# Kernel optimization log

Hardware: AMD Instinct MI355X
Metric: run time of the kernel (lower is better)

## Reference

```python
import jax, jax.numpy as jnp
import numpy as np

N, E = 3072, 49152
C_IN, HID, C_OUT = 16, 64, 3
KS = (2000, 1000, 500)  # ceil(pool_ratio * n_nodes) per depth: 2000/3072, 0.5, 0.5


def gcn(x, A, W, b):
    # GCNConv(improved=True) with edge weights: A_hat = A + 2I,
    # out = D^-1/2 A_hat D^-1/2 (x W) + b
    n = A.shape[0]
    i = jnp.arange(n)
    A_hat = A.at[i, i].add(2.0)
    deg = A_hat.sum(axis=1)
    dis = jnp.where(deg > 0, 1.0 / jnp.sqrt(deg), 0.0)
    return (dis[:, None] * A_hat * dis[None, :]) @ (x @ W) + b


def augment(A):
    # GraphUNet.augment_adj: remove self loops, add self loops (w=1),
    # spspmm(A, A) -> A^2, remove self loops. Dense equivalent.
    n = A.shape[0]
    i = jnp.arange(n)
    A1 = A.at[i, i].set(1.0)
    A2 = A1 @ A1
    return A2.at[i, i].set(0.0)


def topk_pool(x, A, p, k):
    # TopKPooling: score = tanh((x . p)/||p||), keep top-k nodes, scale features
    score = jnp.tanh((x @ p) / jnp.linalg.norm(p))
    _, perm = jax.lax.top_k(score, k)
    x = x[perm] * score[perm][:, None]
    return x, A[perm][:, perm], perm


def setup_inputs():
    key = jax.random.key(0)
    ks = jax.random.split(key, 16)
    g = lambda k, shape, s=1.0: jax.random.normal(k, shape, dtype=jnp.float32) * s
    s = 0.1
    return {
        "x": g(ks[0], (N, C_IN)),
        "edge_index": jax.random.randint(ks[1], (2, E), 0, N),
        "Wd0": g(ks[2], (C_IN, HID), s), "bd0": jnp.zeros((HID,), jnp.float32),
        "Wd1": g(ks[3], (HID, HID), s), "bd1": jnp.zeros((HID,), jnp.float32),
        "Wd2": g(ks[4], (HID, HID), s), "bd2": jnp.zeros((HID,), jnp.float32),
        "Wd3": g(ks[5], (HID, HID), s), "bd3": jnp.zeros((HID,), jnp.float32),
        "p1": g(ks[6], (HID,), s), "p2": g(ks[7], (HID,), s), "p3": g(ks[8], (HID,), s),
        "Wu0": g(ks[9], (HID, HID), s), "bu0": jnp.zeros((HID,), jnp.float32),
        "Wu1": g(ks[10], (HID, HID), s), "bu1": jnp.zeros((HID,), jnp.float32),
        "Wu2": g(ks[11], (HID, C_OUT), s), "bu2": jnp.zeros((C_OUT,), jnp.float32),
    }


def reference(x, edge_index, Wd0, bd0, Wd1, bd1, Wd2, bd2, Wd3, bd3,
              p1, p2, p3, Wu0, bu0, Wu1, bu1, Wu2, bu2):
    # eval mode: dropout_edge(p=0.2) and F.dropout(p=0.92) are identity
    # dense weighted adjacency; duplicate edges sum, matching sparse scatter-add
    A = jnp.zeros((N, N), jnp.float32).at[edge_index[0], edge_index[1]].add(1.0)
    x = jax.nn.relu(gcn(x, A, Wd0, bd0))
    xs, adjs, perms = [x], [A], []
    for i, (W, b, p) in enumerate(((Wd1, bd1, p1), (Wd2, bd2, p2), (Wd3, bd3, p3))):
        A = augment(A)
        x, A, perm = topk_pool(x, A, p, KS[i])
        x = jax.nn.relu(gcn(x, A, W, b))
        if i < 2:
            xs.append(x)
            adjs.append(A)
        perms.append(perm)
    for i, (W, b) in enumerate(((Wu0, bu0), (Wu1, bu1), (Wu2, bu2))):
        j = 2 - i
        res, Aj, perm = xs[j], adjs[j], perms[j]
        up = jnp.zeros_like(res).at[perm].set(x)  # unpool
        x = gcn(res + up, Aj, W, b)  # sum_res=True skip connection
        if i < 2:
            x = jax.nn.relu(x)
    return jax.nn.softmax(x, axis=1)
```

## Files before the change

kernel.cpp:

```cpp
#include <hip/hip_runtime.h>
#include <hip/hip_bf16.h>
#include <cstdint>
#include <cstddef>
#include <math.h>


#define DIVUP(a,b) (((a)+(b)-1)/(b))

using s16x8 = __attribute__((ext_vector_type(8))) short;
using f32x4 = __attribute__((ext_vector_type(4))) float;
using l64x2 = __attribute__((ext_vector_type(2))) long;

template<int N> __device__ __forceinline__ void waitvm() {
    if constexpr (N == 0)       asm volatile("s_waitcnt vmcnt(0)" ::: "memory");
    else if constexpr (N == 2)  asm volatile("s_waitcnt vmcnt(2)" ::: "memory");
    else if constexpr (N == 4)  asm volatile("s_waitcnt vmcnt(4)" ::: "memory");
    else if constexpr (N == 8)  asm volatile("s_waitcnt vmcnt(8)" ::: "memory");
    else                        asm volatile("s_waitcnt vmcnt(16)" ::: "memory");
}

__device__ __forceinline__ unsigned short f2bf(float v) {
    union { float f; unsigned u; } a; a.f = v;
    unsigned u = a.u;
    u = u + 0x7FFFu + ((u >> 16) & 1u);
    return (unsigned short)(u >> 16);
}
__device__ __forceinline__ float bf2f(unsigned short h) {
    union { unsigned u; float f; } a; a.u = ((unsigned)h) << 16; return a.f;
}
__device__ __forceinline__ unsigned char f2e4m3(float v) {
    if (v <= 0.f) return 0;
    int e = 0; float m = v;
    while (m >= 2.f) { m *= 0.5f; ++e; }
    int mant = (int)(m * 8.f + 0.5f) - 8;
    if (mant >= 8) { mant = 0; ++e; }
    return (unsigned char)(((e + 7) << 3) | mant);
}
__device__ __forceinline__ int perm64(int x) {
    return ((x >> 3) & 3) * 16 + ((x >> 5) & 1) * 8 + (x & 7);
}
__device__ __forceinline__ void gload_lds16(const unsigned short* g, unsigned short* l) {
    __builtin_amdgcn_global_load_lds(
        (const __attribute__((address_space(1))) void*)g,
        (__attribute__((address_space(3))) void*)l, 16, 0, 0);
}
__device__ __forceinline__ void gload_lds16b(const unsigned char* g, unsigned char* l) {
    __builtin_amdgcn_global_load_lds(
        (const __attribute__((address_space(1))) void*)g,
        (__attribute__((address_space(3))) void*)l, 16, 0, 0);
}


__global__ void k_scatter(const int* __restrict__ e, float* __restrict__ A, int E, int n) {
    int t = blockIdx.x * blockDim.x + threadIdx.x;
    if (t < E) atomicAdd(&A[(size_t)e[t] * n + e[E + t]], 1.0f);
}

__global__ void k_a0_plane(const float* __restrict__ A, unsigned short* __restrict__ H,
                           unsigned char* __restrict__ F8,
                           float* __restrict__ d0, float* __restrict__ dsum, int n) {
    int t = blockIdx.x * 256 + threadIdx.x;
    int i = t / n, j = t - i * n;
    float v = A[t];
    if (i == j) { d0[i] = v; v = 1.0f; }
    H[t] = f2bf(v);
    F8[(size_t)i * n + (j & ~63) + perm64(j & 63)] = f2e4m3(v);
    __shared__ float red[256];
    red[threadIdx.x] = v; __syncthreads();
    for (int o = 128; o > 0; o >>= 1) {
        if (threadIdx.x < o) red[threadIdx.x] += red[threadIdx.x + o];
        __syncthreads();
    }
    if (threadIdx.x == 0) atomicAdd(&dsum[i], red[0]);
}

__global__ void k_transpose_i8(const unsigned char* __restrict__ S, unsigned char* __restrict__ D, int n) {
    __shared__ unsigned char tile[64][65];
    int bx = blockIdx.x * 64, by = blockIdx.y * 64;
    const int tx = threadIdx.x & 63, ty = threadIdx.x >> 6;
    #pragma unroll
    for (int dy = 0; dy < 64; dy += 4)
        tile[ty + dy][tx] = S[(size_t)(by + ty + dy) * n + bx + perm64(tx)];
    __syncthreads();
    #pragma unroll
    for (int dy = 0; dy < 64; dy += 4)
        D[(size_t)(bx + ty + dy) * n + by + perm64(tx)] = tile[tx][ty + dy];
}

__global__ void k_disv(const float* __restrict__ dsum, const float* __restrict__ diag,
                       float* __restrict__ dis, int n) {
    int i = blockIdx.x * blockDim.x + threadIdx.x;
    if (i >= n) return;
    float deg = dsum[i] + 1.0f + (diag ? diag[i] : 0.0f);
    dis[i] = deg > 0.f ? 1.0f / sqrtf(deg) : 0.f;
}

__global__ void k_scores(const float* __restrict__ x, const float* __restrict__ pv,
                         float* __restrict__ sc, int n) {
    __shared__ float pl[64];
    if (threadIdx.x < 64) pl[threadIdx.x] = pv[threadIdx.x];
    __syncthreads();
    float n2 = 0.f;
    #pragma unroll
    for (int k = 0; k < 64; ++k) n2 += pl[k] * pl[k];
    float nrm = sqrtf(n2);
    int i = blockIdx.x * blockDim.x + threadIdx.x;
    if (i >= n) return;
    const float* xr = x + (size_t)i * 64;
    float d = 0.f;
    #pragma unroll
    for (int k = 0; k < 64; ++k) d += xr[k] * pl[k];
    sc[i] = tanhf(d / nrm);
}

__global__ void k_count_rank(const float* __restrict__ score, int* __restrict__ rank, int n) {
    __shared__ float ls[256];
    const int i = blockIdx.x * 256 + threadIdx.x;
    const int j0 = blockIdx.y * 256;
    int jj_n = n - j0; if (jj_n > 256) jj_n = 256;
    ls[threadIdx.x] = (j0 + threadIdx.x < n) ? score[j0 + threadIdx.x] : -INFINITY;
    __syncthreads();
    if (i >= n) return;
    const float si = score[i];
    int cnt = 0;
    for (int jj = 0; jj < jj_n; ++jj) {
        float sj = ls[jj];
        int j = j0 + jj;
        cnt += (sj > si) || (sj == si && j < i);
    }
    atomicAdd(&rank[i], cnt);
}

__global__ void k_topk_finish(const float* __restrict__ score, const int* __restrict__ rank,
                              const float* __restrict__ x, int n, int k, int kp,
                              int* __restrict__ perm, float* __restrict__ scout,
                              float* __restrict__ xo) {
    int i = blockIdx.x * blockDim.x + threadIdx.x;
    if (i < n) {
        int r = rank[i];
        if (r < k) {
            float s = score[i];
            perm[r] = i; scout[r] = s;
            const float* xr = x + (size_t)i * 64;
            float* xw = xo + (size_t)r * 64;
            #pragma unroll 8
            for (int f = 0; f < 64; ++f) xw[f] = xr[f] * s;
        }
    }
    if (i >= k && i < kp) { perm[i] = 0; scout[i] = 0.f; }
}

__global__ void k_unpool(const float* __restrict__ res, const float* __restrict__ xc,
                         const int* __restrict__ rank, float* __restrict__ o, int n, int k) {
    int t = blockIdx.x * blockDim.x + threadIdx.x;
    if (t >= n * 64) return;
    int r = rank[t >> 6];
    o[t] = res[t] + (r < k ? xc[(size_t)r * 64 + (t & 63)] : 0.f);
}

__global__ void k_xw(const float* __restrict__ x, const float* __restrict__ W,
                     const float* __restrict__ dis, int n, int np, int cin, int ldw, int nout,
                     float* __restrict__ Y, unsigned short* __restrict__ T0,
                     unsigned short* __restrict__ T1, unsigned short* __restrict__ T2) {
    int t = blockIdx.x * blockDim.x + threadIdx.x;
    if (t >= np * 64) return;
    int i = t >> 6, f = t & 63;
    float y = 0.f;
    if (i < n && f < nout) {
        float a = 0.f;
        for (int k = 0; k < cin; ++k) a += x[(size_t)i * cin + k] * W[(size_t)k * ldw + f];
        y = dis[i] * a;
    }
    Y[t] = y;
    unsigned short h0 = f2bf(y);
    float r1 = y - bf2f(h0);
    unsigned short h1 = f2bf(r1);
    float r2 = r1 - bf2f(h1);
    size_t ti = (size_t)f * np + i;
    T0[ti] = h0; T1[ti] = h1; T2[ti] = f2bf(r2);
}


template<int TM>
__global__ __launch_bounds__(256) void k_aug8(
    const unsigned char* __restrict__ P8, const unsigned char* __restrict__ Q8,
    const int* __restrict__ perm, int kk, int kp, int K, int ns,
    unsigned short* __restrict__ H0, unsigned short* __restrict__ T0,
    float* __restrict__ dsum)
{
    constexpr int BM = TM * 32;
    constexpr int PS = BM * 64;
    constexpr int D = 3;
    constexpr int STG = 2 * PS;
    constexpr int LPP = TM / 2;
    constexpr int LPS = 2 * LPP;
    constexpr int TRE = BM * (BM + 2) * 2;
    constexpr int SMEB = (D * STG > TRE) ? D * STG : TRE;
    __shared__ __align__(16) unsigned char smem[SMEB];
    const int tid = threadIdx.x, lane = tid & 63;
    const int wm = tid >> 7, wn = (tid >> 6) & 1;
    const int bm = blockIdx.x * BM, bn = blockIdx.y * BM;
    const unsigned char* spA[LPP];
    const unsigned char* spB[LPP];
    int dstb[LPP];
    #pragma unroll
    for (int it = 0; it < LPP; ++it) {
        int s = tid + it * 256;
        int row = s >> 2, c = (s & 3) ^ ((row >> 1) & 3);
        dstb[it] = (s - lane) * 16;
        spA[it] = P8 + (size_t)perm[bm + row] * ns + 16 * c;
        spB[it] = Q8 + (size_t)perm[bn + row] * ns + 16 * c;
    }
    f32x4 acc[TM][TM] = {};
    const int l15 = lane & 15, kb = lane >> 4;
    const int nt = K >> 6;

    auto stage = [&](int b, int koff) {
        unsigned char* base = smem + b * STG;
        #pragma unroll
        for (int it = 0; it < LPP; ++it) gload_lds16b(spA[it] + koff, base + dstb[it]);
        #pragma unroll
        for (int it = 0; it < LPP; ++it) gload_lds16b(spB[it] + koff, base + PS + dstb[it]);
    };
    auto compute = [&](int b) {
        const unsigned char* base = smem + b * STG;
        l64x2 av[TM], bv[TM];
        #pragma unroll
        for (int mi = 0; mi < TM; ++mi) {
            int row = wm * (TM * 16) + mi * 16 + l15;
            int slot = kb ^ ((row >> 1) & 3);
            av[mi] = *(const l64x2*)(base + row * 64 + slot * 16);
        }
        #pragma unroll
        for (int ni = 0; ni < TM; ++ni) {
            int row = wn * (TM * 16) + ni * 16 + l15;
            int slot = kb ^ ((row >> 1) & 3);
            bv[ni] = *(const l64x2*)(base + PS + row * 64 + slot * 16);
        }
        #pragma unroll
        for (int h = 0; h < 2; ++h)
            #pragma unroll
            for (int mi = 0; mi < TM; ++mi)
                #pragma unroll
                for (int ni = 0; ni < TM; ++ni)
                    acc[mi][ni] = __builtin_amdgcn_mfma_f32_16x16x32_fp8_fp8(
                        av[mi][h], bv[ni][h], acc[mi][ni], 0, 0, 0);
    };

    stage(0, 0); stage(1, 64);
    for (int t = 0; t < nt; ++t) {
        const int ahead = nt - 1 - t;
        if (ahead >= D - 1) {
            stage((t + D - 1) % D, (t + D - 1) * 64);
            waitvm<2 * LPS>();
        } else if (ahead == 1) {
            waitvm<LPS>();
        } else {
            waitvm<0>();
        }
        __builtin_amdgcn_sched_barrier(0);
        __builtin_amdgcn_s_barrier();
        compute(t % D);
        __builtin_amdgcn_s_barrier();
    }

    const int hi = lane >> 4;
    #pragma unroll
    for (int mi = 0; mi < TM; ++mi)
        #pragma unroll
        for (int r = 0; r < 4; ++r) {
            int row = bm + wm * (TM * 16) + mi * 16 + hi * 4 + r;
            float s = 0.f;
            #pragma unroll
            for (int ni = 0; ni < TM; ++ni) {
                int col = bn + wn * (TM * 16) + ni * 16 + l15;
                float v = (row < kk && col < kk) ? ((row == col) ? 1.f : acc[mi][ni][r]) : 0.f;
                H0[(size_t)row * kp + col] = f2bf(v);
                s += v;
            }
            #pragma unroll
            for (int m = 1; m < 16; m <<= 1) s += __shfl_xor(s, m);
            if (l15 == 0) atomicAdd(&dsum[row], s);
        }

    unsigned short* smw = (unsigned short*)smem;
    __syncthreads();
    #pragma unroll
    for (int mi = 0; mi < TM; ++mi)
        #pragma unroll
        for (int ni = 0; ni < TM; ++ni)
            #pragma unroll
            for (int r = 0; r < 4; ++r) {
                int rl = wm * (TM * 16) + mi * 16 + hi * 4 + r;
                int cl = wn * (TM * 16) + ni * 16 + l15;
                int row = bm + rl, col = bn + cl;
                float v = (row < kk && col < kk) ? ((row == col) ? 1.f : acc[mi][ni][r]) : 0.f;
                smw[rl * (BM + 2) + cl] = f2bf(v);
            }
    __syncthreads();
    #pragma unroll
    for (int e = 0; e < BM * BM / 256; ++e) {
        int idx = tid + e * 256;
        int j = idx / BM, i = idx & (BM - 1);
        T0[(size_t)(bn + j) * kp + (bm + i)] = smw[i * (BM + 2) + j];
    }
}

template<int TM, int PA, int PB, int NP, int NT>
__global__ __launch_bounds__(256) void k_aug2(
    const unsigned short* __restrict__ Pa, const unsigned short* __restrict__ Pb,
    const unsigned short* __restrict__ Qa, const unsigned short* __restrict__ Qb,
    const int* __restrict__ perm, int kk, int kp, int K, int ns,
    unsigned short* __restrict__ H0, unsigned short* __restrict__ H1,
    unsigned short* __restrict__ H2,
    unsigned short* __restrict__ T0, unsigned short* __restrict__ T1,
    float* __restrict__ dsum)
{
    constexpr int BM  = TM * 32;
    constexpr int PS  = TM * 2048;
    constexpr int D   = 3;
    constexpr int STG = (PA + PB) * PS;
    constexpr int LPS = TM * (PA + PB);
    constexpr int TRE = NT ? (BM * (BM + 2)) : 0;
    constexpr int SME = (D * STG > TRE) ? (D * STG) : TRE;
    __shared__ __align__(16) unsigned short smem[SME];
    const int tid = threadIdx.x, lane = tid & 63;
    const int wm = tid >> 7, wn = (tid >> 6) & 1;
    const int bm = blockIdx.x * BM, bn = blockIdx.y * BM;
    const unsigned short* P[2] = {Pa, Pb};
    const unsigned short* Q[2] = {Qa, Qb};
    const unsigned short* sp[PA][TM];
    const unsigned short* sq[PB][TM];
    int dst[TM];
    #pragma unroll
    for (int it = 0; it < TM; ++it) {
        int s = tid + it * 256;
        int row = s >> 3, c = (s & 7) ^ (row & 7);
        dst[it] = (s - lane) * 8;
        #pragma unroll
        for (int p = 0; p < PA; ++p)
            sp[p][it] = P[p] + (size_t)perm[bm + row] * ns + 8 * c;
        #pragma unroll
        for (int p = 0; p < PB; ++p)
            sq[p][it] = Q[p] + (size_t)perm[bn + row] * ns + 8 * c;
    }
    f32x4 acc[TM][TM] = {};
    const int l15 = lane & 15, kb = lane >> 4;
    const int nt = K >> 6;

    auto stage = [&](int b, int koff) {
        unsigned short* base = smem + b * STG;
        #pragma unroll
        for (int p = 0; p < PA; ++p)
            #pragma unroll
            for (int it = 0; it < TM; ++it)
                gload_lds16(sp[p][it] + koff, base + p * PS + dst[it]);
        #pragma unroll
        for (int p = 0; p < PB; ++p)
            #pragma unroll
            for (int it = 0; it < TM; ++it)
                gload_lds16(sq[p][it] + koff, base + PA * PS + p * PS + dst[it]);
    };
    auto compute = [&](int b) {
        const unsigned short* base = smem + b * STG;
        #pragma unroll
        for (int h = 0; h < 2; ++h) {
            s16x8 av[PA][TM], bv[PB][TM];
            #pragma unroll
            for (int p = 0; p < PA; ++p)
                #pragma unroll
                for (int mi = 0; mi < TM; ++mi) {
                    int row = wm * (TM * 16) + mi * 16 + l15;
                    int slot = (h * 4 + kb) ^ (row & 7);
                    av[p][mi] = *(const s16x8*)(base + p * PS + row * 64 + slot * 8);
                }
            #pragma unroll
            for (int p = 0; p < PB; ++p)
                #pragma unroll
                for (int ni = 0; ni < TM; ++ni) {
                    int row = wn * (TM * 16) + ni * 16 + l15;
                    int slot = (h * 4 + kb) ^ (row & 7);
                    bv[p][ni] = *(const s16x8*)(base + PA * PS + p * PS + row * 64 + slot * 8);
                }
            #pragma unroll
            for (int mi = 0; mi < TM; ++mi)
                #pragma unroll
                for (int ni = 0; ni < TM; ++ni)
                    #pragma unroll
                    for (int pa = 0; pa < PA; ++pa)
                        #pragma unroll
                        for (int pb = 0; pb < PB; ++pb)
                            acc[mi][ni] = __builtin_amdgcn_mfma_f32_16x16x32_bf16(
                                av[pa][mi], bv[pb][ni], acc[mi][ni], 0, 0, 0);
        }
    };

    for (int i = 0; i < D - 1; ++i) stage(i, i * 64);
    for (int t = 0; t < nt; ++t) {
        const int ahead = nt - 1 - t;
        if (ahead >= D - 1) {
            stage((t + D - 1) % D, (t + D - 1) * 64);
            waitvm<2 * LPS>();
        } else if (ahead == 1) {
            waitvm<LPS>();
        } else {
            waitvm<0>();
        }
        __builtin_amdgcn_sched_barrier(0);
        __builtin_amdgcn_s_barrier();
        compute(t % D);
        __builtin_amdgcn_s_barrier();
    }

    const int hi = lane >> 4;
    #pragma unroll
    for (int mi = 0; mi < TM; ++mi)
        #pragma unroll
        for (int r = 0; r < 4; ++r) {
            int row = bm + wm * (TM * 16) + mi * 16 + hi * 4 + r;
            float s = 0.f;
            #pragma unroll
            for (int ni = 0; ni < TM; ++ni) {
                int col = bn + wn * (TM * 16) + ni * 16 + l15;
                float v = (row < kk && col < kk) ? ((row == col) ? 1.f : acc[mi][ni][r]) : 0.f;
                s += v;
                unsigned short h0 = f2bf(v);
                size_t o = (size_t)row * kp + col;
                H0[o] = h0;
                if (NP > 1) {
                    float r1 = v - bf2f(h0);
                    unsigned short h1 = f2bf(r1);
                    H1[o] = h1;
                    if (NP > 2) H2[o] = f2bf(r1 - bf2f(h1));
                }
            }
            #pragma unroll
            for (int m = 1; m < 16; m <<= 1) s += __shfl_xor(s, m);
            if (l15 == 0) atomicAdd(&dsum[row], s);
        }

    if (NT > 0) {
        #pragma unroll
        for (int pass = 0; pass < NT; ++pass) {
            __syncthreads();
            #pragma unroll
            for (int mi = 0; mi < TM; ++mi)
                #pragma unroll
                for (int ni = 0; ni < TM; ++ni)
                    #pragma unroll
                    for (int r = 0; r < 4; ++r) {
                        int rl = wm * (TM * 16) + mi * 16 + hi * 4 + r;
                        int cl = wn * (TM * 16) + ni * 16 + l15;
                        int row = bm + rl, col = bn + cl;
                        float v = (row < kk && col < kk) ? ((row == col) ? 1.f : acc[mi][ni][r]) : 0.f;
                        unsigned short h0 = f2bf(v);
                        unsigned short hv = h0;
                        if (pass == 1) hv = f2bf(v - bf2f(h0));
                        smem[rl * (BM + 2) + cl] = hv;
                    }
            __syncthreads();
            unsigned short* T = pass ? T1 : T0;
            #pragma unroll
            for (int e = 0; e < BM * BM / 256; ++e) {
                int idx = tid + e * 256;
                int j = idx / BM, i = idx & (BM - 1);
                T[(size_t)(bn + j) * kp + (bm + i)] = smem[i * (BM + 2) + j];
            }
        }
    }
}

template<int PA>
__global__ __launch_bounds__(256) void k_gcn_gemm(
    const unsigned short* __restrict__ Aa, const unsigned short* __restrict__ Ab,
    const unsigned short* __restrict__ Ac,
    const unsigned short* __restrict__ B0, const unsigned short* __restrict__ B1,
    const unsigned short* __restrict__ B2,
    int np, int kchunk, float* __restrict__ Zp)
{
    __shared__ __align__(16) unsigned short la[PA * 4096];
    __shared__ __align__(16) unsigned short lb[3 * 4096];
    const int tid = threadIdx.x, lane = tid & 63, wv = tid >> 6;
    const int bm = blockIdx.x * 64;
    const int kbeg = blockIdx.y * kchunk;
    const unsigned short* A[3] = {Aa, Ab, Ac};
    const unsigned short* B[3] = {B0, B1, B2};
    const unsigned short* sa[PA][2];
    const unsigned short* sb[3][2];
    int dst[2];
    #pragma unroll
    for (int it = 0; it < 2; ++it) {
        int s = tid + it * 256;
        int row = s >> 3, c = (s & 7) ^ (row & 7);
        dst[it] = (s - lane) * 8;
        #pragma unroll
        for (int p = 0; p < PA; ++p)
            sa[p][it] = A[p] + (size_t)(bm + row) * np + kbeg + 8 * c;
        #pragma unroll
        for (int p = 0; p < 3; ++p)
            sb[p][it] = B[p] + (size_t)row * np + kbeg + 8 * c;
    }
    f32x4 acc[4] = {};
    const int l15 = lane & 15, kb = lane >> 4;
    const int nt = kchunk >> 6;

    for (int tt = 0; tt < nt; ++tt) {
        if (tt) __syncthreads();
        int koff = tt * 64;
        #pragma unroll
        for (int p = 0; p < PA; ++p)
            #pragma unroll
            for (int it = 0; it < 2; ++it)
                gload_lds16(sa[p][it] + koff, &la[p * 4096 + dst[it]]);
        #pragma unroll
        for (int p = 0; p < 3; ++p)
            #pragma unroll
            for (int it = 0; it < 2; ++it)
                gload_lds16(sb[p][it] + koff, &lb[p * 4096 + dst[it]]);
        __syncthreads();
        #pragma unroll
        for (int h = 0; h < 2; ++h) {
            s16x8 av[PA], bv[3][4];
            #pragma unroll
            for (int p = 0; p < PA; ++p) {
                int row = wv * 16 + l15;
                int slot = (h * 4 + kb) ^ (row & 7);
                av[p] = *(const s16x8*)&la[p * 4096 + row * 64 + slot * 8];
            }
            #pragma unroll
            for (int p = 0; p < 3; ++p)
                #pragma unroll
                for (int ni = 0; ni < 4; ++ni) {
                    int row = ni * 16 + l15;
                    int slot = (h * 4 + kb) ^ (row & 7);
                    bv[p][ni] = *(const s16x8*)&lb[p * 4096 + row * 64 + slot * 8];
                }
            #pragma unroll
            for (int ni = 0; ni < 4; ++ni)
                #pragma unroll
                for (int pa = 0; pa < PA; ++pa)
                    #pragma unroll
                    for (int pb = 0; pb <= 2 - pa; ++pb)
                        acc[ni] = __builtin_amdgcn_mfma_f32_16x16x32_bf16(
                            av[pa], bv[pb][ni], acc[ni], 0, 0, 0);
        }
    }

    const int l4 = lane >> 4;
    float* Z = Zp + (size_t)blockIdx.y * np * 64;
    for (int ni = 0; ni < 4; ++ni)
        #pragma unroll
        for (int r = 0; r < 4; ++r) {
            int row = bm + wv * 16 + l4 * 4 + r;
            Z[(size_t)row * 64 + ni * 16 + l15] = acc[ni][r];
        }
}

__global__ void k_gcn_epi(const float* __restrict__ Zp, const float* __restrict__ Y,
                          const float* __restrict__ dis, const float* __restrict__ diagv,
                          const float* __restrict__ b, int n, int np, int nout, int relu,
                          int S, float* __restrict__ xo) {
    int t = blockIdx.x * blockDim.x + threadIdx.x;
    if (t >= n * 64) return;
    int i = t >> 6, f = t & 63;
    float s = 0.f;
    for (int kq = 0; kq < S; ++kq) s += Zp[(size_t)kq * np * 64 + t];
    float coef = 1.f + (diagv ? diagv[i] : 0.f);
    float v = dis[i] * (s + coef * Y[t]) + (f < nout ? b[f] : 0.f);
    if (relu) v = fmaxf(v, 0.f);
    xo[t] = v;
}

__global__ void k_softmax(const float* __restrict__ lg, float* __restrict__ o, int n) {
    int i = blockIdx.x * blockDim.x + threadIdx.x;
    if (i >= n) return;
    float a = lg[i * 64], b = lg[i * 64 + 1], c = lg[i * 64 + 2];
    float m = fmaxf(a, fmaxf(b, c));
    float ea = expf(a - m), eb = expf(b - m), ec = expf(c - m);
    float s = ea + eb + ec;
    o[i * 3] = ea / s; o[i * 3 + 1] = eb / s; o[i * 3 + 2] = ec / s;
}


extern "C" void kernel_launch(void* const* d_in, const int* in_sizes, int n_in,
                              void* d_out, int out_size, void* d_ws, size_t ws_size,
                              hipStream_t stream) {
    const int N0 = 3072;
    const int E = in_sizes[1] / 2;
    const int CIN = in_sizes[0] / N0;

    const float* x_in = (const float*)d_in[0];
    const int*   eidx = (const int*)d_in[1];
    const float* Wd0 = (const float*)d_in[2];  const float* bd0 = (const float*)d_in[3];
    const float* Wd1 = (const float*)d_in[4];  const float* bd1 = (const float*)d_in[5];
    const float* Wd2 = (const float*)d_in[6];  const float* bd2 = (const float*)d_in[7];
    const float* Wd3 = (const float*)d_in[8];  const float* bd3 = (const float*)d_in[9];
    const float* p1  = (const float*)d_in[10]; const float* p2  = (const float*)d_in[11];
    const float* p3  = (const float*)d_in[12];
    const float* Wu0 = (const float*)d_in[13]; const float* bu0 = (const float*)d_in[14];
    const float* Wu1 = (const float*)d_in[15]; const float* bu1 = (const float*)d_in[16];
    const float* Wu2 = (const float*)d_in[17]; const float* bu2 = (const float*)d_in[18];
    float* out = (float*)d_out;

    char* ws = (char*)d_ws;
    size_t off = 0;
    auto alloc = [&](size_t bytes) -> void* {
        off = (off + 255) & ~(size_t)255;
        void* p = ws + off;
        off += bytes;
        return p;
    };

    unsigned short* A0H  = (unsigned short*)alloc((size_t)3072 * 3072 * 2);
    unsigned char*  A0F8 = (unsigned char*)alloc((size_t)3072 * 3072);
    unsigned char*  A0T8 = (unsigned char*)alloc((size_t)3072 * 3072);
    float* d0   = (float*)alloc(3072 * 4);
    float* dis0 = (float*)alloc(3072 * 4);
    float* x0   = (float*)alloc((size_t)3072 * 64 * 4);
    unsigned short* P1H = (unsigned short*)alloc((size_t)2048 * 2048 * 2);
    unsigned short* P1T = (unsigned short*)alloc((size_t)2048 * 2048 * 2);
    float* dis1 = (float*)alloc(2048 * 4);
    float* x1   = (float*)alloc((size_t)2048 * 64 * 4);
    float* xp1  = (float*)alloc((size_t)2048 * 64 * 4);
    unsigned short* P2H  = (unsigned short*)alloc((size_t)1024 * 1024 * 2);
    unsigned short* P2L  = (unsigned short*)alloc((size_t)1024 * 1024 * 2);
    unsigned short* P2TH = (unsigned short*)alloc((size_t)1024 * 1024 * 2);
    unsigned short* P2TL = (unsigned short*)alloc((size_t)1024 * 1024 * 2);
    float* dis2 = (float*)alloc(1024 * 4);
    float* x2   = (float*)alloc((size_t)1024 * 64 * 4);
    float* xp2  = (float*)alloc((size_t)1024 * 64 * 4);
    unsigned short* P3a = (unsigned short*)alloc((size_t)512 * 512 * 2);
    unsigned short* P3b = (unsigned short*)alloc((size_t)512 * 512 * 2);
    unsigned short* P3c = (unsigned short*)alloc((size_t)512 * 512 * 2);
    float* dis3 = (float*)alloc(512 * 4);
    float* x3   = (float*)alloc((size_t)512 * 64 * 4);
    float* xp3  = (float*)alloc((size_t)512 * 64 * 4);
    int*   perm1 = (int*)alloc(2048 * 4);  float* sc1 = (float*)alloc(2048 * 4);
    int*   perm2 = (int*)alloc(1024 * 4);  float* sc2 = (float*)alloc(1024 * 4);
    int*   perm3 = (int*)alloc(512 * 4);   float* sc3 = (float*)alloc(512 * 4);
    float* score = (float*)alloc(3072 * 4);
    float* dsum0 = (float*)alloc(3072 * 4);
    float* dsum1 = (float*)alloc(2048 * 4);
    float* dsum2 = (float*)alloc(1024 * 4);
    float* dsum3 = (float*)alloc(512 * 4);
    int* rank1 = (int*)alloc(3072 * 4);
    int* rank2 = (int*)alloc(2048 * 4);
    int* rank3 = (int*)alloc(1024 * 4);
    float* Yf  = (float*)alloc((size_t)3072 * 64 * 4);
    unsigned short* Yt0 = (unsigned short*)alloc((size_t)64 * 3072 * 2);
    unsigned short* Yt1 = (unsigned short*)alloc((size_t)64 * 3072 * 2);
    unsigned short* Yt2 = (unsigned short*)alloc((size_t)64 * 3072 * 2);
    float* Zp   = (float*)alloc((size_t)8 * 3072 * 64 * 4);
    float* xlog = (float*)alloc((size_t)3072 * 64 * 4);
    float* t2b  = (float*)alloc((size_t)1024 * 64 * 4);
    float* t1b  = (float*)alloc((size_t)2048 * 64 * 4);
    float* t0b  = (float*)alloc((size_t)3072 * 64 * 4);
    char* scratch = (char*)alloc((size_t)3072 * 3072 * 4);
    if (off > ws_size) return;

    float* A0f = (float*)scratch;

    auto gcn = [&](const float* xin, int cin, const float* W, int ldw, int nout, const float* bias,
                   const unsigned short* Pa, const unsigned short* Pb2, const unsigned short* Pc,
                   int PA, int n, int np2, const float* dis, const float* diagv, int relu, float* xout) {
        k_xw<<<DIVUP(np2 * 64, 256), 256, 0, stream>>>(xin, W, dis, n, np2, cin, ldw, nout, Yf, Yt0, Yt1, Yt2);
        int S = (np2 == 1024) ? 16 : 8;
        int kch = np2 / S;
        dim3 gg(np2 / 64, S);
        if (PA == 1)      k_gcn_gemm<1><<<gg, 256, 0, stream>>>(Pa, Pa, Pa, Yt0, Yt1, Yt2, np2, kch, Zp);
        else if (PA == 2) k_gcn_gemm<2><<<gg, 256, 0, stream>>>(Pa, Pb2, Pb2, Yt0, Yt1, Yt2, np2, kch, Zp);
        else              k_gcn_gemm<3><<<gg, 256, 0, stream>>>(Pa, Pb2, Pc, Yt0, Yt1, Yt2, np2, kch, Zp);
        k_gcn_epi<<<DIVUP(n * 64, 256), 256, 0, stream>>>(Zp, Yf, dis, diagv, bias, n, np2, nout, relu, S, xout);
    };

    auto topk = [&](const float* x, const float* pvec, int n, int k, int kp,
                    int* rank, int* perm, float* scv, float* xo) {
        k_scores<<<DIVUP(n, 256), 256, 0, stream>>>(x, pvec, score, n);
        dim3 gr(DIVUP(n, 256), DIVUP(n, 256));
        k_count_rank<<<gr, 256, 0, stream>>>(score, rank, n);
        k_topk_finish<<<DIVUP(n, 256), 256, 0, stream>>>(score, rank, x, n, k, kp, perm, scv, xo);
    };

    hipMemsetAsync(dsum0, 0, (char*)(rank3 + 1024) - (char*)dsum0, stream);

    hipMemsetAsync(A0f, 0, (size_t)3072 * 3072 * 4, stream);
    k_scatter<<<DIVUP(E, 256), 256, 0, stream>>>(eidx, A0f, E, N0);
    k_a0_plane<<<3072 * 3072 / 256, 256, 0, stream>>>(A0f, A0H, A0F8, d0, dsum0, N0);
    k_transpose_i8<<<dim3(48, 48), 256, 0, stream>>>(A0F8, A0T8, 3072);
    k_disv<<<DIVUP(3072, 256), 256, 0, stream>>>(dsum0, d0, dis0, 3072);

    gcn(x_in, CIN, Wd0, 64, 64, bd0, A0H, A0H, A0H, 1, 3072, 3072, dis0, d0, 1, x0);

    topk(x0, p1, 3072, 2000, 2048, rank1, perm1, sc1, xp1);
    k_aug8<2><<<dim3(32, 32), 256, 0, stream>>>(
        A0F8, A0T8, perm1, 2000, 2048, 3072, 3072, P1H, P1T, dsum1);
    k_disv<<<DIVUP(2048, 256), 256, 0, stream>>>(dsum1, nullptr, dis1, 2048);
    gcn(xp1, 64, Wd1, 64, 64, bd1, P1H, P1H, P1H, 1, 2000, 2048, dis1, nullptr, 1, x1);

    topk(x1, p2, 2000, 1000, 1024, rank2, perm2, sc2, xp2);
    k_aug2<2, 1, 1, 2, 2><<<dim3(16, 16), 256, 0, stream>>>(
        P1H, P1H, P1T, P1T, perm2, 1000, 1024, 2048, 2048, P2H, P2L, P2L, P2TH, P2TL, dsum2);
    k_disv<<<DIVUP(1024, 256), 256, 0, stream>>>(dsum2, nullptr, dis2, 1024);
    gcn(xp2, 64, Wd2, 64, 64, bd2, P2H, P2L, P2L, 2, 1000, 1024, dis2, nullptr, 1, x2);

    topk(x2, p3, 1000, 500, 512, rank3, perm3, sc3, xp3);
    k_aug2<2, 2, 2, 3, 0><<<dim3(8, 8), 256, 0, stream>>>(
        P2H, P2L, P2TH, P2TL, perm3, 500, 512, 1024, 1024, P3a, P3b, P3c, nullptr, nullptr, dsum3);
    k_disv<<<DIVUP(512, 256), 256, 0, stream>>>(dsum3, nullptr, dis3, 512);
    gcn(xp3, 64, Wd3, 64, 64, bd3, P3a, P3b, P3c, 3, 500, 512, dis3, nullptr, 1, x3);

    k_unpool<<<DIVUP(1000 * 64, 256), 256, 0, stream>>>(x2, x3, rank3, t2b, 1000, 500);
    gcn(t2b, 64, Wu0, 64, 64, bu0, P2H, P2L, P2L, 2, 1000, 1024, dis2, nullptr, 1, xp2);

    k_unpool<<<DIVUP(2000 * 64, 256), 256, 0, stream>>>(x1, xp2, rank2, t1b, 2000, 1000);
    gcn(t1b, 64, Wu1, 64, 64, bu1, P1H, P1H, P1H, 1, 2000, 2048, dis1, nullptr, 1, xp1);

    k_unpool<<<DIVUP(3072 * 64, 256), 256, 0, stream>>>(x0, xp1, rank1, t0b, 3072, 2000);
    gcn(t0b, 64, Wu2, 3, 3, bu2, A0H, A0H, A0H, 1, 3072, 3072, dis0, d0, 0, xlog);

    k_softmax<<<DIVUP(3072, 256), 256, 0, stream>>>(xlog, out, 3072);
}
```

Measured before the change: 393.7 us.

## Fuse score and degree-normalization kernels into consumers, raise GCN split-K to 16

Removes the k_disv launches by computing D^-1/2 inline in k_xw and k_gcn_epi from dsum/diag, and removes k_scores by recomputing the tanh score inside k_count_rank and k_topk_finish. It also raises the split-K factor to 16 for the 2048 and 3072 GCN GEMMs, enlarging the Zp partial buffer. The aim is fewer small kernel launches and better GEMM occupancy, at the cost of redundant dot-product recomputation in the rank kernel and more partial-sum traffic in the epilogue.

```diff
diff --git a/kernel.cpp b/kernel.cpp
--- a/kernel.cpp
+++ b/kernel.cpp
@@ -38,6 +38,10 @@
 }
 __device__ __forceinline__ int perm64(int x) {
     return ((x >> 3) & 3) * 16 + ((x >> 5) & 1) * 8 + (x & 7);
+}
+__device__ __forceinline__ float disv(const float* dsum, const float* diag, int i) {
+    float deg = dsum[i] + 1.0f + (diag ? diag[i] : 0.0f);
+    return deg > 0.f ? 1.0f / sqrtf(deg) : 0.f;
 }
 __device__ __forceinline__ void gload_lds16(const unsigned short* g, unsigned short* l) {
     __builtin_amdgcn_global_load_lds(
@@ -87,61 +91,68 @@
         D[(size_t)(bx + ty + dy) * n + by + perm64(tx)] = tile[tx][ty + dy];
 }
 
-__global__ void k_disv(const float* __restrict__ dsum, const float* __restrict__ diag,
-                       float* __restrict__ dis, int n) {
-    int i = blockIdx.x * blockDim.x + threadIdx.x;
+__global__ void k_count_rank(const float* __restrict__ x, const float* __restrict__ pv,
+                             int* __restrict__ rank, int n) {
+    __shared__ float pl[64];
+    __shared__ float ls[256];
+    if (threadIdx.x < 64) pl[threadIdx.x] = pv[threadIdx.x];
+    __syncthreads();
+    float n2 = 0.f;
+    #pragma unroll
+    for (int k = 0; k < 64; ++k) n2 += pl[k] * pl[k];
+    const float nrm = sqrtf(n2);
+    const int i = blockIdx.x * 256 + threadIdx.x;
+    const int j = blockIdx.y * 256 + threadIdx.x;
+    float sj = -INFINITY;
+    if (j < n) {
+        const float* xr = x + (size_t)j * 64;
+        float d = 0.f;
+        #pragma unroll
+        for (int k = 0; k < 64; ++k) d += xr[k] * pl[k];
+        sj = tanhf(d / nrm);
+    }
+    ls[threadIdx.x] = sj;
+    __syncthreads();
     if (i >= n) return;
-    float deg = dsum[i] + 1.0f + (diag ? diag[i] : 0.0f);
-    dis[i] = deg > 0.f ? 1.0f / sqrtf(deg) : 0.f;
-}
-
-__global__ void k_scores(const float* __restrict__ x, const float* __restrict__ pv,
-                         float* __restrict__ sc, int n) {
+    float si;
+    {
+        const float* xr = x + (size_t)i * 64;
+        float d = 0.f;
+        #pragma unroll
+        for (int k = 0; k < 64; ++k) d += xr[k] * pl[k];
+        si = tanhf(d / nrm);
+    }
+    const int j0 = blockIdx.y * 256;
+    int jj_n = n - j0; if (jj_n > 256) jj_n = 256;
+    int cnt = 0;
+    for (int jj = 0; jj < jj_n; ++jj) {
+        float s2 = ls[jj];
+        cnt += (s2 > si) || (s2 == si && (j0 + jj) < i);
+    }
+    atomicAdd(&rank[i], cnt);
+}
+
+__global__ void k_topk_finish(const float* __restrict__ x, const float* __restrict__ pv,
+                              const int* __restrict__ rank, int n, int k, int kp,
+                              int* __restrict__ perm, float* __restrict__ scout,
+                              float* __restrict__ xo) {
     __shared__ float pl[64];
     if (threadIdx.x < 64) pl[threadIdx.x] = pv[threadIdx.x];
     __syncthreads();
     float n2 = 0.f;
     #pragma unroll
-    for (int k = 0; k < 64; ++k) n2 += pl[k] * pl[k];
-    float nrm = sqrtf(n2);
-    int i = blockIdx.x * blockDim.x + threadIdx.x;
-    if (i >= n) return;
-    const float* xr = x + (size_t)i * 64;
-    float d = 0.f;
-    #pragma unroll
-    for (int k = 0; k < 64; ++k) d += xr[k] * pl[k];
-    sc[i] = tanhf(d / nrm);
-}
-
-__global__ void k_count_rank(const float* __restrict__ score, int* __restrict__ rank, int n) {
-    __shared__ float ls[256];
-    const int i = blockIdx.x * 256 + threadIdx.x;
-    const int j0 = blockIdx.y * 256;
-    int jj_n = n - j0; if (jj_n > 256) jj_n = 256;
-    ls[threadIdx.x] = (j0 + threadIdx.x < n) ? score[j0 + threadIdx.x] : -INFINITY;
-    __syncthreads();
-    if (i >= n) return;
-    const float si = score[i];
-    int cnt = 0;
-    for (int jj = 0; jj < jj_n; ++jj) {
-        float sj = ls[jj];
-        int j = j0 + jj;
-        cnt += (sj > si) || (sj == si && j < i);
-    }
-    atomicAdd(&rank[i], cnt);
-}
-
-__global__ void k_topk_finish(const float* __restrict__ score, const int* __restrict__ rank,
-                              const float* __restrict__ x, int n, int k, int kp,
-                              int* __restrict__ perm, float* __restrict__ scout,
-                              float* __restrict__ xo) {
+    for (int kq = 0; kq < 64; ++kq) n2 += pl[kq] * pl[kq];
+    const float nrm = sqrtf(n2);
     int i = blockIdx.x * blockDim.x + threadIdx.x;
     if (i < n) {
         int r = rank[i];
         if (r < k) {
-            float s = score[i];
+            const float* xr = x + (size_t)i * 64;
+            float d = 0.f;
+            #pragma unroll
+            for (int kq = 0; kq < 64; ++kq) d += xr[kq] * pl[kq];
+            float s = tanhf(d / nrm);
             perm[r] = i; scout[r] = s;
-            const float* xr = x + (size_t)i * 64;
             float* xw = xo + (size_t)r * 64;
             #pragma unroll 8
             for (int f = 0; f < 64; ++f) xw[f] = xr[f] * s;
@@ -159,7 +170,8 @@
 }
 
 __global__ void k_xw(const float* __restrict__ x, const float* __restrict__ W,
-                     const float* __restrict__ dis, int n, int np, int cin, int ldw, int nout,
+                     const float* __restrict__ dsum, const float* __restrict__ diag,
+                     int n, int np, int cin, int ldw, int nout,
                      float* __restrict__ Y, unsigned short* __restrict__ T0,
                      unsigned short* __restrict__ T1, unsigned short* __restrict__ T2) {
     int t = blockIdx.x * blockDim.x + threadIdx.x;
@@ -169,7 +181,7 @@
     if (i < n && f < nout) {
         float a = 0.f;
         for (int k = 0; k < cin; ++k) a += x[(size_t)i * cin + k] * W[(size_t)k * ldw + f];
-        y = dis[i] * a;
+        y = disv(dsum, diag, i) * a;
     }
     Y[t] = y;
     unsigned short h0 = f2bf(y);
@@ -557,7 +569,7 @@
 }
 
 __global__ void k_gcn_epi(const float* __restrict__ Zp, const float* __restrict__ Y,
-                          const float* __restrict__ dis, const float* __restrict__ diagv,
+                          const float* __restrict__ dsum, const float* __restrict__ diagv,
                           const float* __restrict__ b, int n, int np, int nout, int relu,
                           int S, float* __restrict__ xo) {
     int t = blockIdx.x * blockDim.x + threadIdx.x;
@@ -566,7 +578,7 @@
     float s = 0.f;
     for (int kq = 0; kq < S; ++kq) s += Zp[(size_t)kq * np * 64 + t];
     float coef = 1.f + (diagv ? diagv[i] : 0.f);
-    float v = dis[i] * (s + coef * Y[t]) + (f < nout ? b[f] : 0.f);
+    float v = disv(dsum, diagv, i) * (s + coef * Y[t]) + (f < nout ? b[f] : 0.f);
     if (relu) v = fmaxf(v, 0.f);
     xo[t] = v;
 }
@@ -615,30 +627,25 @@
     unsigned char*  A0F8 = (unsigned char*)alloc((size_t)3072 * 3072);
     unsigned char*  A0T8 = (unsigned char*)alloc((size_t)3072 * 3072);
     float* d0   = (float*)alloc(3072 * 4);
-    float* dis0 = (float*)alloc(3072 * 4);
     float* x0   = (float*)alloc((size_t)3072 * 64 * 4);
     unsigned short* P1H = (unsigned short*)alloc((size_t)2048 * 2048 * 2);
     unsigned short* P1T = (unsigned short*)alloc((size_t)2048 * 2048 * 2);
-    float* dis1 = (float*)alloc(2048 * 4);
     float* x1   = (float*)alloc((size_t)2048 * 64 * 4);
     float* xp1  = (float*)alloc((size_t)2048 * 64 * 4);
     unsigned short* P2H  = (unsigned short*)alloc((size_t)1024 * 1024 * 2);
     unsigned short* P2L  = (unsigned short*)alloc((size_t)1024 * 1024 * 2);
     unsigned short* P2TH = (unsigned short*)alloc((size_t)1024 * 1024 * 2);
     unsigned short* P2TL = (unsigned short*)alloc((size_t)1024 * 1024 * 2);
-    float* dis2 = (float*)alloc(1024 * 4);
     float* x2   = (float*)alloc((size_t)1024 * 64 * 4);
     float* xp2  = (float*)alloc((size_t)1024 * 64 * 4);
     unsigned short* P3a = (unsigned short*)alloc((size_t)512 * 512 * 2);
     unsigned short* P3b = (unsigned short*)alloc((size_t)512 * 512 * 2);
     unsigned short* P3c = (unsigned short*)alloc((size_t)512 * 512 * 2);
-    float* dis3 = (float*)alloc(512 * 4);
     float* x3   = (float*)alloc((size_t)512 * 64 * 4);
     float* xp3  = (float*)alloc((size_t)512 * 64 * 4);
     int*   perm1 = (int*)alloc(2048 * 4);  float* sc1 = (float*)alloc(2048 * 4);
     int*   perm2 = (int*)alloc(1024 * 4);  float* sc2 = (float*)alloc(1024 * 4);
     int*   perm3 = (int*)alloc(512 * 4);   float* sc3 = (float*)alloc(512 * 4);
-    float* score = (float*)alloc(3072 * 4);
     float* dsum0 = (float*)alloc(3072 * 4);
     float* dsum1 = (float*)alloc(2048 * 4);
     float* dsum2 = (float*)alloc(1024 * 4);
@@ -650,7 +657,7 @@
     unsigned short* Yt0 = (unsigned short*)alloc((size_t)64 * 3072 * 2);
     unsigned short* Yt1 = (unsigned short*)alloc((size_t)64 * 3072 * 2);
     unsigned short* Yt2 = (unsigned short*)alloc((size_t)64 * 3072 * 2);
-    float* Zp   = (float*)alloc((size_t)8 * 3072 * 64 * 4);
+    float* Zp   = (float*)alloc((size_t)16 * 3072 * 64 * 4);
     float* xlog = (float*)alloc((size_t)3072 * 64 * 4);
     float* t2b  = (float*)alloc((size_t)1024 * 64 * 4);
     float* t1b  = (float*)alloc((size_t)2048 * 64 * 4);
@@ -662,23 +669,22 @@
 
     auto gcn = [&](const float* xin, int cin, const float* W, int ldw, int nout, const float* bias,
                    const unsigned short* Pa, const unsigned short* Pb2, const unsigned short* Pc,
-                   int PA, int n, int np2, const float* dis, const float* diagv, int relu, float* xout) {
-        k_xw<<<DIVUP(np2 * 64, 256), 256, 0, stream>>>(xin, W, dis, n, np2, cin, ldw, nout, Yf, Yt0, Yt1, Yt2);
-        int S = (np2 == 1024) ? 16 : 8;
+                   int PA, int n, int np2, const float* dsum, const float* diagv, int relu, float* xout) {
+        k_xw<<<DIVUP(np2 * 64, 256), 256, 0, stream>>>(xin, W, dsum, diagv, n, np2, cin, ldw, nout, Yf, Yt0, Yt1, Yt2);
+        int S = (np2 >= 1024) ? 16 : 8;
         int kch = np2 / S;
         dim3 gg(np2 / 64, S);
         if (PA == 1)      k_gcn_gemm<1><<<gg, 256, 0, stream>>>(Pa, Pa, Pa, Yt0, Yt1, Yt2, np2, kch, Zp);
         else if (PA == 2) k_gcn_gemm<2><<<gg, 256, 0, stream>>>(Pa, Pb2, Pb2, Yt0, Yt1, Yt2, np2, kch, Zp);
         else              k_gcn_gemm<3><<<gg, 256, 0, stream>>>(Pa, Pb2, Pc, Yt0, Yt1, Yt2, np2, kch, Zp);
-        k_gcn_epi<<<DIVUP(n * 64, 256), 256, 0, stream>>>(Zp, Yf, dis, diagv, bias, n, np2, nout, relu, S, xout);
+        k_gcn_epi<<<DIVUP(n * 64, 256), 256, 0, stream>>>(Zp, Yf, dsum, diagv, bias, n, np2, nout, relu, S, xout);
     };
 
     auto topk = [&](const float* x, const float* pvec, int n, int k, int kp,
                     int* rank, int* perm, float* scv, float* xo) {
-        k_scores<<<DIVUP(n, 256), 256, 0, stream>>>(x, pvec, score, n);
         dim3 gr(DIVUP(n, 256), DIVUP(n, 256));
-        k_count_rank<<<gr, 256, 0, stream>>>(score, rank, n);
-        k_topk_finish<<<DIVUP(n, 256), 256, 0, stream>>>(score, rank, x, n, k, kp, perm, scv, xo);
+        k_count_rank<<<gr, 256, 0, stream>>>(x, pvec, rank, n);
+        k_topk_finish<<<DIVUP(n, 256), 256, 0, stream>>>(x, pvec, rank, n, k, kp, perm, scv, xo);
     };
 
     hipMemsetAsync(dsum0, 0, (char*)(rank3 + 1024) - (char*)dsum0, stream);
@@ -687,36 +693,32 @@
     k_scatter<<<DIVUP(E, 256), 256, 0, stream>>>(eidx, A0f, E, N0);
     k_a0_plane<<<3072 * 3072 / 256, 256, 0, stream>>>(A0f, A0H, A0F8, d0, dsum0, N0);
     k_transpose_i8<<<dim3(48, 48), 256, 0, stream>>>(A0F8, A0T8, 3072);
-    k_disv<<<DIVUP(3072, 256), 256, 0, stream>>>(dsum0, d0, dis0, 3072);
-
-    gcn(x_in, CIN, Wd0, 64, 64, bd0, A0H, A0H, A0H, 1, 3072, 3072, dis0, d0, 1, x0);
+
+    gcn(x_in, CIN, Wd0, 64, 64, bd0, A0H, A0H, A0H, 1, 3072, 3072, dsum0, d0, 1, x0);
 
     topk(x0, p1, 3072, 2000, 2048, rank1, perm1, sc1, xp1);
     k_aug8<2><<<dim3(32, 32), 256, 0, stream>>>(
         A0F8, A0T8, perm1, 2000, 2048, 3072, 3072, P1H, P1T, dsum1);
-    k_disv<<<DIVUP(2048, 256), 256, 0, stream>>>(dsum1, nullptr, dis1, 2048);
-    gcn(xp1, 64, Wd1, 64, 64, bd1, P1H, P1H, P1H, 1, 2000, 2048, dis1, nullptr, 1, x1);
+    gcn(xp1, 64, Wd1, 64, 64, bd1, P1H, P1H, P1H, 1, 2000, 2048, dsum1, nullptr, 1, x1);
 
     topk(x1, p2, 2000, 1000, 1024, rank2, perm2, sc2, xp2);
     k_aug2<2, 1, 1, 2, 2><<<dim3(16, 16), 256, 0, stream>>>(
         P1H, P1H, P1T, P1T, perm2, 1000, 1024, 2048, 2048, P2H, P2L, P2L, P2TH, P2TL, dsum2);
-    k_disv<<<DIVUP(1024, 256), 256, 0, stream>>>(dsum2, nullptr, dis2, 1024);
-    gcn(xp2, 64, Wd2, 64, 64, bd2, P2H, P2L, P2L, 2, 1000, 1024, dis2, nullptr, 1, x2);
+    gcn(xp2, 64, Wd2, 64, 64, bd2, P2H, P2L, P2L, 2, 1000, 1024, dsum2, nullptr, 1, x2);
 
     topk(x2, p3, 1000, 500, 512, rank3, perm3, sc3, xp3);
     k_aug2<2, 2, 2, 3, 0><<<dim3(8, 8), 256, 0, stream>>>(
         P2H, P2L, P2TH, P2TL, perm3, 500, 512, 1024, 1024, P3a, P3b, P3c, nullptr, nullptr, dsum3);
-    k_disv<<<DIVUP(512, 256), 256, 0, stream>>>(dsum3, nullptr, dis3, 512);
-    gcn(xp3, 64, Wd3, 64, 64, bd3, P3a, P3b, P3c, 3, 500, 512, dis3, nullptr, 1, x3);
+    gcn(xp3, 64, Wd3, 64, 64, bd3, P3a, P3b, P3c, 3, 500, 512, dsum3, nullptr, 1, x3);
 
     k_unpool<<<DIVUP(1000 * 64, 256), 256, 0, stream>>>(x2, x3, rank3, t2b, 1000, 500);
-    gcn(t2b, 64, Wu0, 64, 64, bu0, P2H, P2L, P2L, 2, 1000, 1024, dis2, nullptr, 1, xp2);
+    gcn(t2b, 64, Wu0, 64, 64, bu0, P2H, P2L, P2L, 2, 1000, 1024, dsum2, nullptr, 1, xp2);
 
     k_unpool<<<DIVUP(2000 * 64, 256), 256, 0, stream>>>(x1, xp2, rank2, t1b, 2000, 1000);
-    gcn(t1b, 64, Wu1, 64, 64, bu1, P1H, P1H, P1H, 1, 2000, 2048, dis1, nullptr, 1, xp1);
+    gcn(t1b, 64, Wu1, 64, 64, bu1, P1H, P1H, P1H, 1, 2000, 2048, dsum1, nullptr, 1, xp1);
 
     k_unpool<<<DIVUP(3072 * 64, 256), 256, 0, stream>>>(x0, xp1, rank1, t0b, 3072, 2000);
-    gcn(t0b, 64, Wu2, 3, 3, bu2, A0H, A0H, A0H, 1, 3072, 3072, dis0, d0, 0, xlog);
+    gcn(t0b, 64, Wu2, 3, 3, bu2, A0H, A0H, A0H, 1, 3072, 3072, dsum0, d0, 0, xlog);
 
     k_softmax<<<DIVUP(3072, 256), 256, 0, stream>>>(xlog, out, 3072);
 }
```

Result: no change. 399.1 us (+1.4%).
